# Kernel tuning notes

Measured on AMD Instinct MI355X. Metric: run time of the kernel, lower is better.

Reference implementation:

```python
import jax, jax.numpy as jnp
import numpy as np

D_MODEL = 1024
NUM_HEADS = 16
D_LATENT = 256
HEAD_DIM = D_MODEL // NUM_HEADS
B, S = 4, 2048


def setup_inputs() -> dict:
    key = jax.random.key(0)
    ks = jax.random.split(key, 11)
    sc_m = 1.0 / np.sqrt(D_MODEL)
    sc_l = 1.0 / np.sqrt(D_LATENT)
    return {
        "x": jax.random.normal(ks[0], (B, S, D_MODEL), dtype=jnp.float32),
        # weights stored as (in, out); equivalent to torch Linear with W^T
        "Wc": jax.random.normal(ks[1], (D_MODEL, D_LATENT), dtype=jnp.float32) * sc_m,
        "bc": jax.random.normal(ks[2], (D_LATENT,), dtype=jnp.float32) * sc_m,
        "Wk": jax.random.normal(ks[3], (D_LATENT, D_MODEL), dtype=jnp.float32) * sc_l,
        "bk": jax.random.normal(ks[4], (D_MODEL,), dtype=jnp.float32) * sc_l,
        "Wv": jax.random.normal(ks[5], (D_LATENT, D_MODEL), dtype=jnp.float32) * sc_l,
        "bv": jax.random.normal(ks[6], (D_MODEL,), dtype=jnp.float32) * sc_l,
        "Wq": jax.random.normal(ks[7], (D_MODEL, D_MODEL), dtype=jnp.float32) * sc_m,
        "bq": jax.random.normal(ks[8], (D_MODEL,), dtype=jnp.float32) * sc_m,
        "Wo": jax.random.normal(ks[9], (D_MODEL, D_MODEL), dtype=jnp.float32) * sc_m,
        "bo": jax.random.normal(ks[10], (D_MODEL,), dtype=jnp.float32) * sc_m,
    }


def reference(x, Wc, bc, Wk, bk, Wv, bv, Wq, bq, Wo, bo):
    b, s, _ = x.shape
    Q = x @ Wq + bq                       # [b,s,d_model]
    kv_latent = x @ Wc + bc               # [b,s,d_latent]
    K = kv_latent @ Wk + bk               # [b,s,d_model]
    V = kv_latent @ Wv + bv               # [b,s,d_model]
    # split heads -> [b,h,s,hd]
    Q = Q.reshape(b, s, NUM_HEADS, HEAD_DIM).transpose(0, 2, 1, 3)
    K = K.reshape(b, s, NUM_HEADS, HEAD_DIM).transpose(0, 2, 1, 3)
    V = V.reshape(b, s, NUM_HEADS, HEAD_DIM).transpose(0, 2, 1, 3)
    scores = jnp.einsum("bhqd,bhkd->bhqk", Q, K) / np.sqrt(HEAD_DIM)
    attn = jax.nn.softmax(scores, axis=-1)  # dropout p=0.0 (eval) -> identity
    out = jnp.einsum("bhqk,bhkd->bhqd", attn, V)
    out = out.transpose(0, 2, 1, 3).reshape(b, s, D_MODEL)
    return out @ Wo + bo
```

## Files before the change

### kernel.cpp

```cpp
#include <hip/hip_runtime.h>

typedef __bf16 bf16;
typedef __bf16 bf16x8 __attribute__((ext_vector_type(8)));
typedef float f32x4 __attribute__((ext_vector_type(4)));

#define NHEADS 16
#define HDIM 64
#define SEQ 2048
#define BATCH 4
#define DMODEL 1024
#define NTOK (BATCH * SEQ)
#define KVBLK 64
#define QSCALE 0.18033688f
#define C0EXP  -28.853901f

typedef void gvoid __attribute__((address_space(1)));
typedef void lvoid __attribute__((address_space(3)));

__device__ __forceinline__ f32x4 mfma16(bf16x8 a, bf16x8 b, f32x4 c) {
  return __builtin_amdgcn_mfma_f32_16x16x32_bf16(a, b, c, 0, 0, 0);
}

__device__ __forceinline__ void gload16(const bf16* g, bf16* l) {
  __builtin_amdgcn_global_load_lds((gvoid*)g, (lvoid*)l, 16, 0, 0);
}

__global__ __launch_bounds__(256) void cvt_f32_bf16(
    const float* __restrict__ in, bf16* __restrict__ out, long n) {
  const long i = ((long)blockIdx.x * 256 + threadIdx.x) * 8;
  if (i >= n) return;
  const float4 a = *(const float4*)(in + i);
  const float4 b = *(const float4*)(in + i + 4);
  bf16x8 o;
  o[0] = (bf16)a.x; o[1] = (bf16)a.y; o[2] = (bf16)a.z; o[3] = (bf16)a.w;
  o[4] = (bf16)b.x; o[5] = (bf16)b.y; o[6] = (bf16)b.z; o[7] = (bf16)b.w;
  *(bf16x8*)(out + i) = o;
}

__global__ __launch_bounds__(256) void transpose_cvt(
    const float* __restrict__ in, bf16* __restrict__ out, int K, int N) {
  __shared__ float t[32][33];
  const int n0 = blockIdx.x * 32, k0 = blockIdx.y * 32;
  for (int i = threadIdx.y; i < 32; i += 8)
    t[i][threadIdx.x] = in[(long)(k0 + i) * N + n0 + threadIdx.x];
  __syncthreads();
  for (int i = threadIdx.y; i < 32; i += 8)
    out[(long)(n0 + i) * K + k0 + threadIdx.x] = (bf16)t[threadIdx.x][i];
}

template <int MODE, typename OutT>
__global__ __launch_bounds__(256) void gemm_bt(
    const bf16* __restrict__ A, const bf16* __restrict__ Bt,
    const float* __restrict__ bias, const float* __restrict__ bias2,
    OutT* __restrict__ D, bf16* __restrict__ D2, int N, int K) {
  __shared__ bf16 As[128 * 32];
  __shared__ bf16 Bs[128 * 32];
  const int tid = threadIdx.x;
  const int lane = tid & 63;
  const int wave = tid >> 6;
  const int wr = (wave >> 1) * 64;
  const int wc = (wave & 1) * 64;
  const int r16 = lane & 15;
  const int kg = lane >> 4;
  const long rowBase = (long)blockIdx.x * 128;
  const long colBase = (long)blockIdx.y * 128;

  const int o0 = tid * 16;
  const int o1 = o0 + 4096;
  const int ra0 = o0 >> 6, ca0 = (o0 & 63) >> 1;
  const int ra1 = o1 >> 6, ca1 = (o1 & 63) >> 1;
  const bf16* pA0 = A + (rowBase + ra0) * K + ca0;
  const bf16* pA1 = A + (rowBase + ra1) * K + ca1;
  const bf16* pB0 = Bt + (colBase + ra0) * K + ca0;
  const bf16* pB1 = Bt + (colBase + ra1) * K + ca1;
  bf16* lA0 = As + (o0 >> 1);
  bf16* lA1 = As + (o1 >> 1);
  bf16* lB0 = Bs + (o0 >> 1);
  bf16* lB1 = Bs + (o1 >> 1);

  f32x4 acc[4][4] = {};

  const int nk = K >> 5;
  for (int kt = 0; kt < nk; ++kt) {
    gload16(pA0, lA0);
    gload16(pA1, lA1);
    gload16(pB0, lB0);
    gload16(pB1, lB1);
    pA0 += 32; pA1 += 32; pB0 += 32; pB1 += 32;
    __syncthreads();
    bf16x8 af[4], bfr[4];
#pragma unroll
    for (int m = 0; m < 4; ++m)
      af[m] = *(const bf16x8*)(As + (wr + m * 16 + r16) * 32 + kg * 8);
#pragma unroll
    for (int n = 0; n < 4; ++n)
      bfr[n] = *(const bf16x8*)(Bs + (wc + n * 16 + r16) * 32 + kg * 8);
#pragma unroll
    for (int m = 0; m < 4; ++m)
#pragma unroll
      for (int n = 0; n < 4; ++n)
        acc[m][n] = mfma16(af[m], bfr[n], acc[m][n]);
    __syncthreads();
  }

#pragma unroll
  for (int n = 0; n < 4; ++n) {
    const long col = colBase + wc + n * 16 + r16;
    const bool primary = (MODE == 0) || (col < 1024);
    const float bvv = primary ? bias[col] : bias2[col - 1024];
#pragma unroll
    for (int m = 0; m < 4; ++m) {
      const long row0 = rowBase + wr + m * 16 + kg * 4;
#pragma unroll
      for (int r = 0; r < 4; ++r) {
        const long row = row0 + r;
        float v = acc[m][n][r] + bvv;
        if (MODE == 0) {
          D[row * N + col] = (OutT)v;
        } else {
          const long b = row >> 11, s = row & (SEQ - 1);
          if (MODE == 3) {
            if (primary) {
              const long h = col >> 6, d = col & 63;
              D[((b * NHEADS + h) * SEQ + s) * HDIM + d] = (OutT)(v * QSCALE);
            } else {
              D2[row * 256 + (col - 1024)] = (bf16)v;
            }
          } else {
            if (primary) {
              const long h = col >> 6, d = col & 63;
              D[((b * NHEADS + h) * SEQ + s) * HDIM + d] = (OutT)v;
            } else {
              const long c2 = col - 1024;
              const long h = c2 >> 6, d = c2 & 63;
              D2[((b * NHEADS + h) * HDIM + d) * SEQ + s] = (bf16)v;
            }
          }
        }
      }
    }
  }
}

__global__ __launch_bounds__(512, 4) void mla_attn(
    const bf16* __restrict__ Q, const bf16* __restrict__ Kg,
    const bf16* __restrict__ Vt, bf16* __restrict__ Out) {
  __shared__ bf16 Kl[2][KVBLK * HDIM];
  __shared__ bf16 Vl[2][HDIM * KVBLK];
  __shared__ bf16 Pl[8][32][72];
  const int tid = threadIdx.x;
  const int lane = tid & 63;
  const int w = tid >> 6;
  const int r16 = lane & 15;
  const int kg = lane >> 4;
  const int qb = blockIdx.x & 7;
  const int bh = blockIdx.x >> 3;
  const bf16* Qp = Q + (long)bh * SEQ * HDIM;
  const bf16* Kp = Kg + (long)bh * SEQ * HDIM;
  const bf16* Vp = Vt + (long)bh * HDIM * SEQ;
  const int q0 = qb * 256 + w * 32;

  const int so = tid * 16;
  const int srow = so >> 7;
  const int scol = ((so & 127) ^ ((srow & 7) << 4)) >> 1;
  const bf16* KgS = Kp + (long)srow * HDIM + scol;
  const bf16* VgS = Vp + (long)srow * SEQ + scol;
  bf16* KlS = (bf16*)Kl[0] + (so >> 1);
  bf16* VlS = (bf16*)Vl[0] + (so >> 1);

  bf16x8 aq[2][2];
#pragma unroll
  for (int qm = 0; qm < 2; ++qm) {
    const bf16* qp = Qp + (long)(q0 + qm * 16 + r16) * HDIM + kg * 8;
    aq[qm][0] = *(const bf16x8*)qp;
    aq[qm][1] = *(const bf16x8*)(qp + 32);
  }

  f32x4 accO[2][4];
  float lsum[2][4];
#pragma unroll
  for (int qm = 0; qm < 2; ++qm) {
#pragma unroll
    for (int r = 0; r < 4; ++r) lsum[qm][r] = 0.f;
#pragma unroll
    for (int dt = 0; dt < 4; ++dt) accO[qm][dt] = (f32x4){0.f, 0.f, 0.f, 0.f};
  }

  auto kaddr = [](const bf16* base, int row, int bytecol) -> const bf16* {
    return base + row * 64 + ((bytecol ^ ((row & 7) << 4)) >> 1);
  };

  gload16(KgS, KlS);
  gload16(VgS, VlS);
  __syncthreads();

  const int NT = SEQ / KVBLK;
  for (int t = 0; t < NT; ++t) {
    const int cur = t & 1;
    if (t + 1 < NT) {
      const long off = (long)(t + 1) * KVBLK;
      gload16(KgS + off * HDIM, KlS + (cur ^ 1) * (KVBLK * HDIM));
      gload16(VgS + off, VlS + (cur ^ 1) * (HDIM * KVBLK));
    }
    f32x4 sc[2][4];
    __builtin_amdgcn_s_setprio(1);
#pragma unroll
    for (int kt = 0; kt < 4; ++kt) {
      const int row = kt * 16 + r16;
      const bf16x8 kf0 = *(const bf16x8*)kaddr(Kl[cur], row, kg * 16);
      const bf16x8 kf1 = *(const bf16x8*)kaddr(Kl[cur], row, 64 + kg * 16);
#pragma unroll
      for (int qm = 0; qm < 2; ++qm) {
        f32x4 tv = (f32x4){C0EXP, C0EXP, C0EXP, C0EXP};
        tv = mfma16(aq[qm][0], kf0, tv);
        tv = mfma16(aq[qm][1], kf1, tv);
        sc[qm][kt] = tv;
      }
    }
    __builtin_amdgcn_s_setprio(0);
#pragma unroll
    for (int qm = 0; qm < 2; ++qm)
#pragma unroll
      for (int r = 0; r < 4; ++r) {
        float ps = 0.f;
#pragma unroll
        for (int kt = 0; kt < 4; ++kt) {
          const float pv = __builtin_amdgcn_exp2f(sc[qm][kt][r]);
          Pl[w][qm * 16 + kg * 4 + r][kt * 16 + r16] = (bf16)pv;
          ps += pv;
        }
        lsum[qm][r] += ps;
      }
    __builtin_amdgcn_s_setprio(1);
#pragma unroll
    for (int kc = 0; kc < 2; ++kc) {
      bf16x8 ap[2];
      ap[0] = *(const bf16x8*)(&Pl[w][r16][kc * 32 + kg * 8]);
      ap[1] = *(const bf16x8*)(&Pl[w][16 + r16][kc * 32 + kg * 8]);
#pragma unroll
      for (int dt = 0; dt < 4; ++dt) {
        const int vrow = dt * 16 + r16;
        const bf16x8 vf = *(const bf16x8*)kaddr(Vl[cur], vrow, kc * 64 + kg * 16);
        accO[0][dt] = mfma16(ap[0], vf, accO[0][dt]);
        accO[1][dt] = mfma16(ap[1], vf, accO[1][dt]);
      }
    }
    __builtin_amdgcn_s_setprio(0);
    __syncthreads();
  }

  const int b = bh >> 4, h = bh & 15;
#pragma unroll
  for (int qm = 0; qm < 2; ++qm)
#pragma unroll
    for (int r = 0; r < 4; ++r) {
      float s = lsum[qm][r];
#pragma unroll
      for (int off = 1; off < 16; off <<= 1) s += __shfl_xor(s, off);
      const float inv = 1.f / s;
      const long qrow = q0 + qm * 16 + kg * 4 + r;
      bf16* op = Out + ((long)b * SEQ + qrow) * DMODEL + h * HDIM;
#pragma unroll
      for (int dt = 0; dt < 4; ++dt)
        op[dt * 16 + r16] = (bf16)(accO[qm][dt][r] * inv);
    }
}

extern "C" void kernel_launch(void* const* d_in, const int* in_sizes, int n_in,
                              void* d_out, int out_size, void* d_ws, size_t ws_size,
                              hipStream_t stream) {
  const float* x  = (const float*)d_in[0];
  const float* Wc = (const float*)d_in[1];
  const float* bc = (const float*)d_in[2];
  const float* Wk = (const float*)d_in[3];
  const float* bk = (const float*)d_in[4];
  const float* Wv = (const float*)d_in[5];
  const float* bv = (const float*)d_in[6];
  const float* Wq = (const float*)d_in[7];
  const float* bq = (const float*)d_in[8];
  const float* Wo = (const float*)d_in[9];
  const float* bo = (const float*)d_in[10];
  float* out = (float*)d_out;

  bf16* p = (bf16*)d_ws;
  bf16* xb   = p; p += (long)NTOK * 1024;
  bf16* WqcT = p; p += 1280 * 1024;
  bf16* WkvT = p; p += 2048 * 256;
  bf16* WoT  = p; p += 1024 * 1024;
  bf16* Qb   = p; p += (long)NTOK * 1024;
  bf16* Kb   = p; p += (long)NTOK * 1024;
  bf16* Vtb  = p; p += (long)NTOK * 1024;
  bf16* Cb   = p; p += (long)NTOK * 256;
  bf16* AO   = xb;

  cvt_f32_bf16<<<(long)NTOK * 1024 / (256 * 8), 256, 0, stream>>>(x, xb, (long)NTOK * 1024);

  dim3 tt(32, 8);
  transpose_cvt<<<dim3(32, 32), tt, 0, stream>>>(Wq, WqcT, 1024, 1024);
  transpose_cvt<<<dim3(8, 32),  tt, 0, stream>>>(Wc, WqcT + 1024 * 1024, 1024, 256);
  transpose_cvt<<<dim3(32, 8),  tt, 0, stream>>>(Wk, WkvT, 256, 1024);
  transpose_cvt<<<dim3(32, 8),  tt, 0, stream>>>(Wv, WkvT + 1024 * 256, 256, 1024);
  transpose_cvt<<<dim3(32, 32), tt, 0, stream>>>(Wo, WoT, 1024, 1024);

  gemm_bt<3, bf16><<<dim3(64, 10), 256, 0, stream>>>(xb, WqcT, bq, bc, Qb, Cb, 1280, 1024);
  gemm_bt<4, bf16><<<dim3(64, 16), 256, 0, stream>>>(Cb, WkvT, bk, bv, Kb, Vtb, 2048, 256);

  mla_attn<<<(SEQ / 256) * BATCH * NHEADS, 512, 0, stream>>>(Qb, Kb, Vtb, AO);

  gemm_bt<0, float><<<dim3(64, 8), 256, 0, stream>>>(AO, WoT, bo, bo, out, (bf16*)nullptr, 1024, 1024);
}
```

Baseline: 209.4 us.

## Triple-buffer GEMM and attention LDS loads with manual waitcnt/barrier pipelining

Both the GEMM and attention kernels move from double or single buffering to a 3-stage LDS ring. Loads are issued two tiles ahead, and the per-iteration double __syncthreads is replaced by explicit vmcnt waits plus a single s_barrier, so global latency overlaps with MFMA work. In attention, the softmax row sum is now computed with an MFMA against a ones vector instead of scalar adds and shuffles, and the P tile drops its padding in favour of an XOR swizzle. The cost is more LDS per block, which may cut occupancy for the 512-thread attention blocks, and correctness now depends on the hand-written waitcnt counts.

Result: faster. 200.5 us (-4.2%).

```diff
diff --git a/kernel.cpp b/kernel.cpp
--- a/kernel.cpp
+++ b/kernel.cpp
@@ -53,8 +53,8 @@
     const bf16* __restrict__ A, const bf16* __restrict__ Bt,
     const float* __restrict__ bias, const float* __restrict__ bias2,
     OutT* __restrict__ D, bf16* __restrict__ D2, int N, int K) {
-  __shared__ bf16 As[128 * 32];
-  __shared__ bf16 Bs[128 * 32];
+  __shared__ bf16 As[3][128 * 32];
+  __shared__ bf16 Bs[3][128 * 32];
   const int tid = threadIdx.x;
   const int lane = tid & 63;
   const int wave = tid >> 6;
@@ -73,35 +73,52 @@
   const bf16* pA1 = A + (rowBase + ra1) * K + ca1;
   const bf16* pB0 = Bt + (colBase + ra0) * K + ca0;
   const bf16* pB1 = Bt + (colBase + ra1) * K + ca1;
-  bf16* lA0 = As + (o0 >> 1);
-  bf16* lA1 = As + (o1 >> 1);
-  bf16* lB0 = Bs + (o0 >> 1);
-  bf16* lB1 = Bs + (o1 >> 1);
+  const int e0 = o0 >> 1, e1 = o1 >> 1;
 
   f32x4 acc[4][4] = {};
-
   const int nk = K >> 5;
+
+#define GSTAGE(kt_)                                        \
+  {                                                        \
+    const int b_ = (kt_) % 3;                              \
+    const int o_ = (kt_) * 32;                             \
+    gload16(pA0 + o_, &As[b_][e0]);                        \
+    gload16(pA1 + o_, &As[b_][e1]);                        \
+    gload16(pB0 + o_, &Bs[b_][e0]);                        \
+    gload16(pB1 + o_, &Bs[b_][e1]);                        \
+  }
+
+  GSTAGE(0);
+  GSTAGE(1);
+  asm volatile("s_waitcnt vmcnt(4)" ::: "memory");
+  asm volatile("s_barrier" ::: "memory");
+
   for (int kt = 0; kt < nk; ++kt) {
-    gload16(pA0, lA0);
-    gload16(pA1, lA1);
-    gload16(pB0, lB0);
-    gload16(pB1, lB1);
-    pA0 += 32; pA1 += 32; pB0 += 32; pB1 += 32;
-    __syncthreads();
+    if (kt + 2 < nk) {
+      GSTAGE(kt + 2);
+      asm volatile("s_waitcnt vmcnt(4)" ::: "memory");
+    } else {
+      asm volatile("s_waitcnt vmcnt(0)" ::: "memory");
+    }
+    const bf16* as = As[kt % 3];
+    const bf16* bs = Bs[kt % 3];
     bf16x8 af[4], bfr[4];
 #pragma unroll
     for (int m = 0; m < 4; ++m)
-      af[m] = *(const bf16x8*)(As + (wr + m * 16 + r16) * 32 + kg * 8);
+      af[m] = *(const bf16x8*)(as + (wr + m * 16 + r16) * 32 + kg * 8);
 #pragma unroll
     for (int n = 0; n < 4; ++n)
-      bfr[n] = *(const bf16x8*)(Bs + (wc + n * 16 + r16) * 32 + kg * 8);
+      bfr[n] = *(const bf16x8*)(bs + (wc + n * 16 + r16) * 32 + kg * 8);
+    __builtin_amdgcn_s_setprio(1);
 #pragma unroll
     for (int m = 0; m < 4; ++m)
 #pragma unroll
       for (int n = 0; n < 4; ++n)
         acc[m][n] = mfma16(af[m], bfr[n], acc[m][n]);
-    __syncthreads();
-  }
+    __builtin_amdgcn_s_setprio(0);
+    asm volatile("s_barrier" ::: "memory");
+  }
+#undef GSTAGE
 
 #pragma unroll
   for (int n = 0; n < 4; ++n) {
@@ -145,9 +162,9 @@
 __global__ __launch_bounds__(512, 4) void mla_attn(
     const bf16* __restrict__ Q, const bf16* __restrict__ Kg,
     const bf16* __restrict__ Vt, bf16* __restrict__ Out) {
-  __shared__ bf16 Kl[2][KVBLK * HDIM];
-  __shared__ bf16 Vl[2][HDIM * KVBLK];
-  __shared__ bf16 Pl[8][32][72];
+  __shared__ bf16 Kl[3][KVBLK * HDIM];
+  __shared__ bf16 Vl[3][HDIM * KVBLK];
+  __shared__ bf16 Pl[8][32][64];
   const int tid = threadIdx.x;
   const int lane = tid & 63;
   const int w = tid >> 6;
@@ -165,8 +182,7 @@
   const int scol = ((so & 127) ^ ((srow & 7) << 4)) >> 1;
   const bf16* KgS = Kp + (long)srow * HDIM + scol;
   const bf16* VgS = Vp + (long)srow * SEQ + scol;
-  bf16* KlS = (bf16*)Kl[0] + (so >> 1);
-  bf16* VlS = (bf16*)Vl[0] + (so >> 1);
+  const int se = so >> 1;
 
   bf16x8 aq[2][2];
 #pragma unroll
@@ -176,43 +192,55 @@
     aq[qm][1] = *(const bf16x8*)(qp + 32);
   }
 
+  bf16x8 kones;
+#pragma unroll
+  for (int j = 0; j < 8; ++j) kones[j] = (bf16)1.0f;
+
   f32x4 accO[2][4];
-  float lsum[2][4];
-#pragma unroll
-  for (int qm = 0; qm < 2; ++qm) {
-#pragma unroll
-    for (int r = 0; r < 4; ++r) lsum[qm][r] = 0.f;
+  f32x4 lsumv[2] = {{0.f, 0.f, 0.f, 0.f}, {0.f, 0.f, 0.f, 0.f}};
+#pragma unroll
+  for (int qm = 0; qm < 2; ++qm)
 #pragma unroll
     for (int dt = 0; dt < 4; ++dt) accO[qm][dt] = (f32x4){0.f, 0.f, 0.f, 0.f};
-  }
+  const f32x4 c0v = {C0EXP, C0EXP, C0EXP, C0EXP};
 
   auto kaddr = [](const bf16* base, int row, int bytecol) -> const bf16* {
     return base + row * 64 + ((bytecol ^ ((row & 7) << 4)) >> 1);
   };
 
-  gload16(KgS, KlS);
-  gload16(VgS, VlS);
-  __syncthreads();
+#define ASTAGE(t_)                                                   \
+  {                                                                  \
+    const int b_ = (t_) % 3;                                         \
+    const long off_ = (long)(t_) * KVBLK;                            \
+    gload16(KgS + off_ * HDIM, (bf16*)Kl[b_] + se);                  \
+    gload16(VgS + off_, (bf16*)Vl[b_] + se);                         \
+  }
+
+  ASTAGE(0);
+  ASTAGE(1);
+  asm volatile("s_waitcnt vmcnt(2)" ::: "memory");
+  asm volatile("s_barrier" ::: "memory");
 
   const int NT = SEQ / KVBLK;
   for (int t = 0; t < NT; ++t) {
-    const int cur = t & 1;
-    if (t + 1 < NT) {
-      const long off = (long)(t + 1) * KVBLK;
-      gload16(KgS + off * HDIM, KlS + (cur ^ 1) * (KVBLK * HDIM));
-      gload16(VgS + off, VlS + (cur ^ 1) * (HDIM * KVBLK));
-    }
+    if (t + 2 < NT) {
+      ASTAGE(t + 2);
+      asm volatile("s_waitcnt vmcnt(2)" ::: "memory");
+    } else {
+      asm volatile("s_waitcnt vmcnt(0)" ::: "memory");
+    }
+    const bf16* kl = Kl[t % 3];
+    const bf16* vl = Vl[t % 3];
     f32x4 sc[2][4];
     __builtin_amdgcn_s_setprio(1);
 #pragma unroll
     for (int kt = 0; kt < 4; ++kt) {
       const int row = kt * 16 + r16;
-      const bf16x8 kf0 = *(const bf16x8*)kaddr(Kl[cur], row, kg * 16);
-      const bf16x8 kf1 = *(const bf16x8*)kaddr(Kl[cur], row, 64 + kg * 16);
+      const bf16x8 kf0 = *(const bf16x8*)kaddr(kl, row, kg * 16);
+      const bf16x8 kf1 = *(const bf16x8*)kaddr(kl, row, 64 + kg * 16);
 #pragma unroll
       for (int qm = 0; qm < 2; ++qm) {
-        f32x4 tv = (f32x4){C0EXP, C0EXP, C0EXP, C0EXP};
-        tv = mfma16(aq[qm][0], kf0, tv);
+        f32x4 tv = mfma16(aq[qm][0], kf0, c0v);
         tv = mfma16(aq[qm][1], kf1, tv);
         sc[qm][kt] = tv;
       }
@@ -222,42 +250,42 @@
     for (int qm = 0; qm < 2; ++qm)
 #pragma unroll
       for (int r = 0; r < 4; ++r) {
-        float ps = 0.f;
+        const int prow = qm * 16 + kg * 4 + r;
+        const int sw = ((kg * 4 + r) & 7) << 3;
 #pragma unroll
         for (int kt = 0; kt < 4; ++kt) {
           const float pv = __builtin_amdgcn_exp2f(sc[qm][kt][r]);
-          Pl[w][qm * 16 + kg * 4 + r][kt * 16 + r16] = (bf16)pv;
-          ps += pv;
+          Pl[w][prow][(kt * 16 + r16) ^ sw] = (bf16)pv;
         }
-        lsum[qm][r] += ps;
       }
     __builtin_amdgcn_s_setprio(1);
 #pragma unroll
     for (int kc = 0; kc < 2; ++kc) {
+      const int psw = (r16 & 7) << 3;
       bf16x8 ap[2];
-      ap[0] = *(const bf16x8*)(&Pl[w][r16][kc * 32 + kg * 8]);
-      ap[1] = *(const bf16x8*)(&Pl[w][16 + r16][kc * 32 + kg * 8]);
+      ap[0] = *(const bf16x8*)(&Pl[w][r16][(kc * 32 + kg * 8) ^ psw]);
+      ap[1] = *(const bf16x8*)(&Pl[w][16 + r16][(kc * 32 + kg * 8) ^ psw]);
+      lsumv[0] = mfma16(ap[0], kones, lsumv[0]);
+      lsumv[1] = mfma16(ap[1], kones, lsumv[1]);
 #pragma unroll
       for (int dt = 0; dt < 4; ++dt) {
         const int vrow = dt * 16 + r16;
-        const bf16x8 vf = *(const bf16x8*)kaddr(Vl[cur], vrow, kc * 64 + kg * 16);
+        const bf16x8 vf = *(const bf16x8*)kaddr(vl, vrow, kc * 64 + kg * 16);
         accO[0][dt] = mfma16(ap[0], vf, accO[0][dt]);
         accO[1][dt] = mfma16(ap[1], vf, accO[1][dt]);
       }
     }
     __builtin_amdgcn_s_setprio(0);
-    __syncthreads();
-  }
+    asm volatile("s_barrier" ::: "memory");
+  }
+#undef ASTAGE
 
   const int b = bh >> 4, h = bh & 15;
 #pragma unroll
   for (int qm = 0; qm < 2; ++qm)
 #pragma unroll
     for (int r = 0; r < 4; ++r) {
-      float s = lsum[qm][r];
-#pragma unroll
-      for (int off = 1; off < 16; off <<= 1) s += __shfl_xor(s, off);
-      const float inv = 1.f / s;
+      const float inv = 1.f / lsumv[qm][r];
       const long qrow = q0 + qm * 16 + kg * 4 + r;
       bf16* op = Out + ((long)b * SEQ + qrow) * DMODEL + h * HDIM;
 #pragma unroll
```
